# Optimization experiments

Measured on AMD Instinct MI355X. Metric: run time of the kernel, lower is better.

Reference implementation:

```python
import jax, jax.numpy as jnp
import numpy as np

B, L, D, C = 4, 512, 128, 128
EPS = 1e-7  # Keras backend epsilon


def setup_inputs() -> dict:
    key = jax.random.key(0)
    ks = jax.random.split(key, 4)
    inps = jax.random.normal(ks[0], (B, L, D), dtype=jnp.float32)
    # glorot_normal-ish scale for weights
    wei_t = jax.random.normal(ks[1], (D, C), dtype=jnp.float32) * (2.0 / (D + C)) ** 0.5
    wei_x = jax.random.normal(ks[2], (D, C), dtype=jnp.float32) * (2.0 / (D + C)) ** 0.5
    bxh = jnp.zeros((C,), dtype=jnp.float32)
    wei_a = jax.random.normal(ks[3], (C,), dtype=jnp.float32) * (2.0 / (C + 1)) ** 0.5
    bxa = jnp.zeros((), dtype=jnp.float32)
    return {"inps": inps, "wei_t": wei_t, "wei_x": wei_x, "bxh": bxh,
            "wei_a": wei_a, "bxa": bxa}


def reference(inps, wei_t, wei_x, bxh, wei_a, bxa):
    # Additive (Bahdanau-style) pairwise self-attention, no mask.
    qt = inps @ wei_t                      # [B, L, C] (query-side projection)
    kx = inps @ wei_x                      # [B, L, C] (key-side projection)
    # Pairwise hidden: [B, L, L, C]
    h = jnp.tanh(qt[:, :, None, :] + kx[:, None, :, :] + bxh)
    scores = jnp.einsum('bijc,c->bij', h, wei_a) + bxa  # [B, L, L]
    # activation_func=None -> linear (identity)
    e = jnp.exp(scores - jnp.max(scores, axis=-1, keepdims=True))
    a = e / (jnp.sum(e, axis=-1, keepdims=True) + EPS)   # [B, L, L]
    out = jnp.einsum('bij,bjd->bid', a, inps)            # [B, L, D]
    return out
```

## Files before the change

### kernel.cpp

```cpp
#include <hip/hip_runtime.h>

#define NB 4
#define SL 512
#define DD 128
#define CC 128

__device__ __forceinline__ float fexp2(float x) { return __builtin_amdgcn_exp2f(x); }
__device__ __forceinline__ float frcp(float x)  { return __builtin_amdgcn_rcpf(x); }

__global__ __launch_bounds__(256) void proj_kernel(
    const float* __restrict__ inps, const float* __restrict__ wei_t,
    const float* __restrict__ wei_x, const float* __restrict__ bxh,
    float* __restrict__ E, float* __restrict__ F)
{
    const float K2 = 2.8853900817779268f;
    const int row0 = blockIdx.x * 2;
    const int b    = row0 >> 9;
    const int i0   = row0 & 511;
    const int c    = threadIdx.x & 127;
    const int sel  = threadIdx.x >> 7;

    const float* W  = sel ? wei_x : wei_t;
    const float* r0 = inps + (size_t)row0 * DD;
    const float* r1 = r0 + DD;

    float a0 = 0.f, a1 = 0.f;
    #pragma unroll 8
    for (int k = 0; k < DD; ++k) {
        float w = W[k * CC + c];
        a0 = fmaf(r0[k], w, a0);
        a1 = fmaf(r1[k], w, a1);
    }

    if (sel == 0) {
        float bb = bxh[c];
        E[(size_t)(row0 + 0) * CC + c] = fexp2(K2 * (a0 + bb));
        E[(size_t)(row0 + 1) * CC + c] = fexp2(K2 * (a1 + bb));
    } else {
        float2 v = {fexp2(K2 * a0), fexp2(K2 * a1)};
        *reinterpret_cast<float2*>(&F[((size_t)b * CC + c) * SL + i0]) = v;
    }
}

__global__ __launch_bounds__(512, 4) void attn_kernel(
    const float* __restrict__ inps, const float* __restrict__ wei_a,
    const float* __restrict__ E, const float* __restrict__ F,
    float* __restrict__ out)
{
    __shared__ float4 upk[CC];
    __shared__ float scT[SL * 4];
    __shared__ float redw[4 * 8];
    __shared__ float redbuf[4 * 16 * DD];

    const int blk = blockIdx.x;
    const int b   = blk >> 7;
    const int i0  = (blk & 127) * 4;
    const int bi0 = b * SL + i0;
    const int tid = threadIdx.x;
    const int j   = tid;
    const int lane = tid & 63, wv = tid >> 6;

    if (tid < CC) {
        float4 u;
        u.x = E[(size_t)(bi0 + 0) * CC + tid];
        u.y = E[(size_t)(bi0 + 1) * CC + tid];
        u.z = E[(size_t)(bi0 + 2) * CC + tid];
        u.w = E[(size_t)(bi0 + 3) * CC + tid];
        upk[tid] = u;
    }
    __syncthreads();

    const float* fb = F + (size_t)b * CC * SL + j;
    float s0 = 0.f, s1 = 0.f, s2 = 0.f, s3 = 0.f;
    #pragma unroll 8
    for (int c = 0; c < CC; ++c) {
        float fv = fb[(size_t)c * SL];
        float4 u = upk[c];
        float wc = wei_a[c];
        s0 = fmaf(wc, frcp(fmaf(u.x, fv, 1.0f)), s0);
        s1 = fmaf(wc, frcp(fmaf(u.y, fv, 1.0f)), s1);
        s2 = fmaf(wc, frcp(fmaf(u.z, fv, 1.0f)), s2);
        s3 = fmaf(wc, frcp(fmaf(u.w, fv, 1.0f)), s3);
    }

    const float KE = -2.8853900817779268f;
    float e0 = fexp2(s0 * KE), e1 = fexp2(s1 * KE);
    float e2 = fexp2(s2 * KE), e3 = fexp2(s3 * KE);
    float t0 = e0, t1 = e1, t2 = e2, t3 = e3;
    #pragma unroll
    for (int off = 32; off > 0; off >>= 1) {
        t0 += __shfl_xor(t0, off, 64);
        t1 += __shfl_xor(t1, off, 64);
        t2 += __shfl_xor(t2, off, 64);
        t3 += __shfl_xor(t3, off, 64);
    }
    if (lane == 0) {
        redw[0 * 8 + wv] = t0; redw[1 * 8 + wv] = t1;
        redw[2 * 8 + wv] = t2; redw[3 * 8 + wv] = t3;
    }
    __syncthreads();
    {
        float S0 = 0.f, S1 = 0.f, S2 = 0.f, S3 = 0.f;
        #pragma unroll
        for (int q = 0; q < 8; ++q) {
            S0 += redw[0 * 8 + q]; S1 += redw[1 * 8 + q];
            S2 += redw[2 * 8 + q]; S3 += redw[3 * 8 + q];
        }
        float4 av = {e0 * frcp(S0 + 1e-7f), e1 * frcp(S1 + 1e-7f),
                     e2 * frcp(S2 + 1e-7f), e3 * frcp(S3 + 1e-7f)};
        *reinterpret_cast<float4*>(&scT[j * 4]) = av;
    }
    __syncthreads();

    const int dq = (tid & 31) * 4;
    const int jq = tid >> 5;
    const float* ibase = inps + (size_t)b * SL * DD;
    float4 acc0 = {0,0,0,0}, acc1 = {0,0,0,0}, acc2 = {0,0,0,0}, acc3 = {0,0,0,0};
    const int jb = jq * 32;
    #pragma unroll 4
    for (int jj = 0; jj < 32; ++jj) {
        int jx = jb + jj;
        float4 v  = *reinterpret_cast<const float4*>(ibase + (size_t)jx * DD + dq);
        float4 a4 = *reinterpret_cast<const float4*>(&scT[jx * 4]);
        acc0.x = fmaf(a4.x, v.x, acc0.x); acc0.y = fmaf(a4.x, v.y, acc0.y);
        acc0.z = fmaf(a4.x, v.z, acc0.z); acc0.w = fmaf(a4.x, v.w, acc0.w);
        acc1.x = fmaf(a4.y, v.x, acc1.x); acc1.y = fmaf(a4.y, v.y, acc1.y);
        acc1.z = fmaf(a4.y, v.z, acc1.z); acc1.w = fmaf(a4.y, v.w, acc1.w);
        acc2.x = fmaf(a4.z, v.x, acc2.x); acc2.y = fmaf(a4.z, v.y, acc2.y);
        acc2.z = fmaf(a4.z, v.z, acc2.z); acc2.w = fmaf(a4.z, v.w, acc2.w);
        acc3.x = fmaf(a4.w, v.x, acc3.x); acc3.y = fmaf(a4.w, v.y, acc3.y);
        acc3.z = fmaf(a4.w, v.z, acc3.z); acc3.w = fmaf(a4.w, v.w, acc3.w);
    }
    *reinterpret_cast<float4*>(&redbuf[(0 * 16 + jq) * DD + dq]) = acc0;
    *reinterpret_cast<float4*>(&redbuf[(1 * 16 + jq) * DD + dq]) = acc1;
    *reinterpret_cast<float4*>(&redbuf[(2 * 16 + jq) * DD + dq]) = acc2;
    *reinterpret_cast<float4*>(&redbuf[(3 * 16 + jq) * DD + dq]) = acc3;
    __syncthreads();
    {
        int i = tid >> 7, d = tid & 127;
        float sum = 0.f;
        #pragma unroll
        for (int q = 0; q < 16; ++q) sum += redbuf[(i * 16 + q) * DD + d];
        out[(size_t)(bi0 + i) * DD + d] = sum;
    }
}

extern "C" void kernel_launch(void* const* d_in, const int* in_sizes, int n_in,
                              void* d_out, int out_size, void* d_ws, size_t ws_size,
                              hipStream_t stream) {
    const float* inps  = (const float*)d_in[0];
    const float* wei_t = (const float*)d_in[1];
    const float* wei_x = (const float*)d_in[2];
    const float* bxh   = (const float*)d_in[3];
    const float* wei_a = (const float*)d_in[4];
    float* out = (float*)d_out;

    float* E = (float*)d_ws;
    float* F = E + (size_t)NB * SL * CC;

    proj_kernel<<<NB * SL / 2, 256, 0, stream>>>(inps, wei_t, wei_x, bxh, E, F);
    attn_kernel<<<NB * SL / 4, 512, 0, stream>>>(inps, wei_a, E, F, out);
}
```

Measured before the change: 95.43 us.

## Merge reciprocal pairs and split channel reduction across thread halves

Combines two tanh-derived reciprocal terms into one reciprocal of a product, halving transcendental rcp ops in the score loop. Each thread now computes two key positions over half the channels, with the halves merged through shared memory before softmax. This adds shared-memory traffic, an extra barrier, and a risk of overflow in the product of two large exponentials; barriers are also placed inside divergent branches.

```diff
diff --git a/kernel.cpp b/kernel.cpp
--- a/kernel.cpp
+++ b/kernel.cpp
@@ -48,8 +48,9 @@
     float* __restrict__ out)
 {
     __shared__ float4 upk[CC];
+    __shared__ float smrg[256 * 9];
     __shared__ float scT[SL * 4];
-    __shared__ float redw[4 * 8];
+    __shared__ float redw[4 * 4];
     __shared__ float redbuf[4 * 16 * DD];
 
     const int blk = blockIdx.x;
@@ -57,8 +58,9 @@
     const int i0  = (blk & 127) * 4;
     const int bi0 = b * SL + i0;
     const int tid = threadIdx.x;
-    const int j   = tid;
-    const int lane = tid & 63, wv = tid >> 6;
+    const int jt  = tid & 255;
+    const int ch  = tid >> 8;
+    const int j0  = jt * 2;
 
     if (tid < CC) {
         float4 u;
@@ -70,45 +72,75 @@
     }
     __syncthreads();
 
-    const float* fb = F + (size_t)b * CC * SL + j;
-    float s0 = 0.f, s1 = 0.f, s2 = 0.f, s3 = 0.f;
-    #pragma unroll 8
-    for (int c = 0; c < CC; ++c) {
-        float fv = fb[(size_t)c * SL];
-        float4 u = upk[c];
-        float wc = wei_a[c];
-        s0 = fmaf(wc, frcp(fmaf(u.x, fv, 1.0f)), s0);
-        s1 = fmaf(wc, frcp(fmaf(u.y, fv, 1.0f)), s1);
-        s2 = fmaf(wc, frcp(fmaf(u.z, fv, 1.0f)), s2);
-        s3 = fmaf(wc, frcp(fmaf(u.w, fv, 1.0f)), s3);
+    const int c0 = ch * 64;
+    const float* fb = F + ((size_t)b * CC + c0) * SL + j0;
+    const float4* up = upk + c0;
+    const float* wa = wei_a + c0;
+    float sx[4] = {0.f, 0.f, 0.f, 0.f};
+    float sy[4] = {0.f, 0.f, 0.f, 0.f};
+    #pragma unroll 4
+    for (int cp = 0; cp < 32; ++cp) {
+        float2 f0 = *reinterpret_cast<const float2*>(&fb[(size_t)(2 * cp) * SL]);
+        float2 f1 = *reinterpret_cast<const float2*>(&fb[(size_t)(2 * cp + 1) * SL]);
+        float4 u0 = up[2 * cp];
+        float4 u1 = up[2 * cp + 1];
+        float wa0 = wa[2 * cp], wa1 = wa[2 * cp + 1];
+        const float* u0p = reinterpret_cast<const float*>(&u0);
+        const float* u1p = reinterpret_cast<const float*>(&u1);
+        #pragma unroll
+        for (int i = 0; i < 4; ++i) {
+            float ax = fmaf(u0p[i], f0.x, 1.0f);
+            float bx = fmaf(u1p[i], f1.x, 1.0f);
+            float numx = fmaf(wa0, bx, wa1 * ax);
+            sx[i] = fmaf(numx, frcp(ax * bx), sx[i]);
+            float ay = fmaf(u0p[i], f0.y, 1.0f);
+            float by = fmaf(u1p[i], f1.y, 1.0f);
+            float numy = fmaf(wa0, by, wa1 * ay);
+            sy[i] = fmaf(numy, frcp(ay * by), sy[i]);
+        }
     }
 
-    const float KE = -2.8853900817779268f;
-    float e0 = fexp2(s0 * KE), e1 = fexp2(s1 * KE);
-    float e2 = fexp2(s2 * KE), e3 = fexp2(s3 * KE);
-    float t0 = e0, t1 = e1, t2 = e2, t3 = e3;
-    #pragma unroll
-    for (int off = 32; off > 0; off >>= 1) {
-        t0 += __shfl_xor(t0, off, 64);
-        t1 += __shfl_xor(t1, off, 64);
-        t2 += __shfl_xor(t2, off, 64);
-        t3 += __shfl_xor(t3, off, 64);
-    }
-    if (lane == 0) {
-        redw[0 * 8 + wv] = t0; redw[1 * 8 + wv] = t1;
-        redw[2 * 8 + wv] = t2; redw[3 * 8 + wv] = t3;
+    if (ch == 1) {
+        #pragma unroll
+        for (int i = 0; i < 4; ++i) {
+            smrg[jt * 9 + i]     = sx[i];
+            smrg[jt * 9 + 4 + i] = sy[i];
+        }
     }
     __syncthreads();
-    {
-        float S0 = 0.f, S1 = 0.f, S2 = 0.f, S3 = 0.f;
+
+    if (ch == 0) {
+        const float KE = -2.8853900817779268f;
+        float ex[4], ey[4];
+        const int lane = tid & 63, wv = tid >> 6;
         #pragma unroll
-        for (int q = 0; q < 8; ++q) {
-            S0 += redw[0 * 8 + q]; S1 += redw[1 * 8 + q];
-            S2 += redw[2 * 8 + q]; S3 += redw[3 * 8 + q];
+        for (int i = 0; i < 4; ++i) {
+            float si = sx[i] + smrg[jt * 9 + i];
+            float ti = sy[i] + smrg[jt * 9 + 4 + i];
+            ex[i] = fexp2(si * KE);
+            ey[i] = fexp2(ti * KE);
+            float t = ex[i] + ey[i];
+            #pragma unroll
+            for (int off = 32; off > 0; off >>= 1)
+                t += __shfl_xor(t, off, 64);
+            if (lane == 0) redw[i * 4 + wv] = t;
         }
-        float4 av = {e0 * frcp(S0 + 1e-7f), e1 * frcp(S1 + 1e-7f),
-                     e2 * frcp(S2 + 1e-7f), e3 * frcp(S3 + 1e-7f)};
-        *reinterpret_cast<float4*>(&scT[j * 4]) = av;
+        __syncthreads();
+        float4 av0, av1;
+        {
+            float S0 = redw[0] + redw[1] + redw[2] + redw[3];
+            float S1 = redw[4] + redw[5] + redw[6] + redw[7];
+            float S2 = redw[8] + redw[9] + redw[10] + redw[11];
+            float S3 = redw[12] + redw[13] + redw[14] + redw[15];
+            float r0 = frcp(S0 + 1e-7f), r1 = frcp(S1 + 1e-7f);
+            float r2 = frcp(S2 + 1e-7f), r3 = frcp(S3 + 1e-7f);
+            av0 = make_float4(ex[0] * r0, ex[1] * r1, ex[2] * r2, ex[3] * r3);
+            av1 = make_float4(ey[0] * r0, ey[1] * r1, ey[2] * r2, ey[3] * r3);
+        }
+        *reinterpret_cast<float4*>(&scT[j0 * 4])     = av0;
+        *reinterpret_cast<float4*>(&scT[j0 * 4 + 4]) = av1;
+    } else {
+        __syncthreads();
     }
     __syncthreads();
 
```

Result: faster. 91.01 us (-4.6%).
